# Performance work log

Hardware: AMD Instinct MI355X
Metric: run time of the kernel (lower is better)

The kernel has to match this reference:

```python
import jax, jax.numpy as jnp
import numpy as np

C64 = jnp.complex64
INV_SQRT2 = 1.0 / np.sqrt(2.0)
_H = jnp.array([[INV_SQRT2, INV_SQRT2], [INV_SQRT2, -INV_SQRT2]], dtype=C64)
_CNOT = jnp.array([[1, 0, 0, 0], [0, 1, 0, 0], [0, 0, 0, 1], [0, 0, 1, 0]], dtype=C64)  # wire0=control (index = 2*b0 + b1)


def _rz(t):
    # diag(e^{-it/2}, e^{it/2})
    return jnp.diag(jnp.stack([jnp.exp(-0.5j * t), jnp.exp(0.5j * t)]))


def _ry(t):
    c, s = jnp.cos(0.5 * t), jnp.sin(0.5 * t)
    return jnp.stack([jnp.stack([c, -s]), jnp.stack([s, c])]).astype(C64)


def _phase(p):
    # diag(1, e^{ip})
    return jnp.diag(jnp.stack([jnp.ones((), C64), jnp.exp(1j * p)]))


def _layer_unitary(p):
    # p: [14] already clipped. Gate order: CNOT -> H x H -> PhaseShift -> Rot(r,0,phi_s)=RZ(r+phi_s)
    #   -> Rot(r,phi_d,0)=RY(phi_d)@RZ(r) -> CPhase(k0)*CPhase(k1) = diag(1,1,1,e^{i(k0+k1)}).
    # bs_theta (p[0]) and bs_phi (p[1]) are computed but never used in a gate, matching the source.
    P = jnp.kron(_phase(p[2]), _phase(p[3]))
    S = jnp.kron(_rz(p[4] + p[6]), _rz(p[5] + p[7]))
    D = jnp.kron(_ry(p[10]) @ _rz(p[8]), _ry(p[11]) @ _rz(p[9]))
    CP = jnp.diag(jnp.stack([jnp.ones((), C64), jnp.ones((), C64), jnp.ones((), C64),
                             jnp.exp(1j * (p[12] + p[13]))]))
    HH = jnp.kron(_H, _H)
    return CP @ D @ S @ P @ HH @ _CNOT


def _total_unitary(params):
    # params: [L, 14]. FraudLayerParameters.__post_init__ clips everything to +-5 (kerr to +-1).
    p = jnp.concatenate([jnp.clip(params[:, :12], -5.0, 5.0),
                         jnp.clip(params[:, 12:], -1.0, 1.0)], axis=1)
    U = jnp.eye(4, dtype=C64)
    for i in range(params.shape[0]):  # static, tiny layer count
        U = _layer_unitary(p[i]) @ U
    return U


def setup_inputs() -> dict:
    key = jax.random.key(0)
    k1, k2, k3, k4 = jax.random.split(key, 4)
    B, n_layers, n_classes = 4194304, 3, 1  # layer 0 = input layer, layers 1..2 = variational
    x = jax.random.normal(k1, (B, 2), dtype=jnp.float32)
    params = jax.random.uniform(k2, (n_layers, 14), dtype=jnp.float32, minval=-1.0, maxval=1.0)
    W = jax.random.normal(k3, (n_classes, 1), dtype=jnp.float32)
    b = jax.random.normal(k4, (n_classes,), dtype=jnp.float32)
    return {"x": x, "params": params, "W": W, "b": b}


def reference(x, params, W, b):
    U = _total_unitary(params)  # constant 4x4 (params don't depend on the sample)
    h = 0.5 * x
    c, s = jnp.cos(h), jnp.sin(h)
    # RX(t)|0> = [cos(t/2), -i sin(t/2)]
    a0 = jnp.stack([c[:, 0].astype(C64), (-1j) * s[:, 0].astype(C64)], axis=-1)  # [B,2]
    a1 = jnp.stack([c[:, 1].astype(C64), (-1j) * s[:, 1].astype(C64)], axis=-1)  # [B,2]
    state = (a0[:, :, None] * a1[:, None, :]).reshape(-1, 4)  # kron, index = 2*b0 + b1
    psi = state @ U.T  # [B,4] = einsum('ij,bj->bi')
    prob = jnp.real(psi * jnp.conj(psi))  # [B,4]
    z_sign = jnp.array([1.0, 1.0, -1.0, -1.0], dtype=jnp.float32)  # <Z on wire 0>
    logits = (prob @ z_sign)[:, None]  # [B,1]
    return logits @ W.T + b  # [B, n_classes]
```

## Files before the change

kernel.cpp:

```cpp
#include <hip/hip_runtime.h>
#include <math.h>


__device__ inline void delem(float r, float phid, int a, int b,
                             float& outr, float& outi) {
    float sn, cs; __sincosf(0.5f * r, &sn, &cs);
    float sd, cd; __sincosf(0.5f * phid, &sd, &cd);
    float f = (a == b) ? cd : ((a == 1) ? sd : -sd);
    outr = f * cs;
    outi = f * ((b == 1) ? sn : -sn);
}

__device__ inline void cmatmul_shfl(float Ar, float Ai, float Br, float Bi,
                                    int i, int j, float& Cr, float& Ci) {
    float cr = 0.f, ci = 0.f;
    #pragma unroll
    for (int k = 0; k < 4; ++k) {
        float ar = __shfl(Ar, 4 * i + k, 64);
        float ai = __shfl(Ai, 4 * i + k, 64);
        float br = __shfl(Br, 4 * k + j, 64);
        float bi = __shfl(Bi, 4 * k + j, 64);
        cr = fmaf(ar, br, fmaf(-ai, bi, cr));
        ci = fmaf(ar, bi, fmaf(ai, br, ci));
    }
    Cr = cr; Ci = ci;
}

__device__ inline float eval_sample(float x0, float x1,
                                    float k00, float k01, float k02,
                                    float k10, float k11, float k12,
                                    float k20, float k21, float k22) {
    float s0, c0, s1, c1;
    __sincosf(x0, &s0, &c0);
    __sincosf(x1, &s1, &c1);
    float e0 = fmaf(s1, k02, fmaf(c1, k01, k00));
    float e1 = fmaf(s1, k12, fmaf(c1, k11, k10));
    float e2 = fmaf(s1, k22, fmaf(c1, k21, k20));
    return fmaf(s0, e2, fmaf(c0, e1, e0));
}

__global__ __launch_bounds__(256) void fraud_fused(
        const float* __restrict__ params, int n_layers,
        const float* __restrict__ W, const float* __restrict__ bias,
        const float4* __restrict__ x, float4* __restrict__ out, int nquads) {
    __shared__ float Am[16];

    const int t = threadIdx.x;

    if (t < 64) {
        const int i = (t >> 2) & 3, j = t & 3;
        const int i0 = i >> 1, i1 = i & 1, j0 = j >> 1, j1 = j & 1;

        float Ur = (i == j) ? 1.f : 0.f, Ui = 0.f;

        for (int l = 0; l < n_layers; ++l) {
            float p[14];
            #pragma unroll
            for (int q = 0; q < 14; ++q) {
                float v = params[l * 14 + q];
                float lim = (q < 12) ? 5.0f : 1.0f;
                p[q] = fminf(fmaxf(v, -lim), lim);
            }

            int sj = j ^ (j >> 1);
            float hh = (__popc(i & sj) & 1) ? -0.5f : 0.5f;
            float t0 = p[4] + p[6], t1 = p[5] + p[7];
            float th = p[2] * (float)i0 + p[3] * (float)i1
                     + 0.5f * t0 * (float)(2 * i0 - 1)
                     + 0.5f * t1 * (float)(2 * i1 - 1);
            float sth, cth; __sincosf(th, &sth, &cth);
            float Er = hh * cth, Ei = hh * sth;

            float ar, ai, br, bi;
            delem(p[8], p[10], i0, j0, ar, ai);
            delem(p[9], p[11], i1, j1, br, bi);
            float D4r = ar * br - ai * bi;
            float D4i = ar * bi + ai * br;

            float Lr, Li;
            cmatmul_shfl(D4r, D4i, Er, Ei, i, j, Lr, Li);
            if (i == 3) {
                float cps, cpc; __sincosf(p[12] + p[13], &cps, &cpc);
                float nr = Lr * cpc - Li * cps;
                float ni = Lr * cps + Li * cpc;
                Lr = nr; Li = ni;
            }

            if (l == 0) { Ur = Lr; Ui = Li; }
            else {
                float nr, ni;
                cmatmul_shfl(Lr, Li, Ur, Ui, i, j, nr, ni);
                Ur = nr; Ui = ni;
            }
        }

        float mr = 0.f, mi = 0.f;
        #pragma unroll
        for (int k = 0; k < 4; ++k) {
            float z = (k < 2) ? 1.f : -1.f;
            float u1r =  __shfl(Ur, 4 * k + i, 64);
            float u1i = -__shfl(Ui, 4 * k + i, 64);
            float u2r =  __shfl(Ur, 4 * k + j, 64);
            float u2i =  __shfl(Ui, 4 * k + j, 64);
            mr += z * (u1r * u2r - u1i * u2i);
            mi += z * (u1r * u2i + u1i * u2r);
        }
        float dri = (i == 0) ? 1.f : ((i == 3) ? -1.f : 0.f);
        float dii = (i == 0 || i == 3) ? 0.f : -1.f;
        float drj = (j == 0) ? 1.f : ((j == 3) ? -1.f : 0.f);
        float dij = (j == 0 || j == 3) ? 0.f : -1.f;
        float fr = dri * drj + dii * dij;
        float fi = dri * dij - dii * drj;
        if (t < 16) Am[t] = mr * fr - mi * fi;
    }
    __syncthreads();

    float A00 = Am[0],  A01 = Am[1],  A02 = Am[2],  A03 = Am[3];
    float A11 = Am[5],  A12 = Am[6],  A13 = Am[7];
    float A22 = Am[10], A23 = Am[11], A33 = Am[15];
    float w = W[0], bb = bias[0];
    float k00 = 0.25f * (A00 + A11 + A22 + A33) * w + bb;
    float k01 = 0.25f * (A00 - A11 + A22 - A33) * w;
    float k02 = 0.5f  * (A01 + A23) * w;
    float k10 = 0.25f * (A00 + A11 - A22 - A33) * w;
    float k11 = 0.25f * (A00 - A11 - A22 + A33) * w;
    float k12 = 0.5f  * (A01 - A23) * w;
    float k20 = 0.5f  * (A02 + A13) * w;
    float k21 = 0.5f  * (A02 - A13) * w;
    float k22 = 0.5f  * (A03 + A12) * w;

    const int gsize = gridDim.x * 256;
    for (int q = blockIdx.x * 256 + t; q < nquads; q += gsize) {
        float4 xa = x[2 * q];
        float4 xb = x[2 * q + 1];
        float4 o;
        o.x = eval_sample(xa.x, xa.y, k00, k01, k02, k10, k11, k12, k20, k21, k22);
        o.y = eval_sample(xa.z, xa.w, k00, k01, k02, k10, k11, k12, k20, k21, k22);
        o.z = eval_sample(xb.x, xb.y, k00, k01, k02, k10, k11, k12, k20, k21, k22);
        o.w = eval_sample(xb.z, xb.w, k00, k01, k02, k10, k11, k12, k20, k21, k22);
        out[q] = o;
    }
}

extern "C" void kernel_launch(void* const* d_in, const int* in_sizes, int n_in,
                              void* d_out, int out_size, void* d_ws, size_t ws_size,
                              hipStream_t stream) {
    const float* x      = (const float*)d_in[0];
    const float* params = (const float*)d_in[1];
    const float* W      = (const float*)d_in[2];
    const float* b      = (const float*)d_in[3];
    float* out = (float*)d_out;

    int n_layers = in_sizes[1] / 14;
    int B = out_size;
    int nq = B / 4;

    int blocks = 2048;
    int maxb = (nq + 255) / 256;
    if (blocks > maxb) blocks = maxb;

    fraud_fused<<<blocks, 256, 0, stream>>>(params, n_layers, W, b,
                                            (const float4*)x, (float4*)out, nq);
}
```

Before: 15.18 us.

## Prefetch first two sample quads before unitary setup and drop one shuffle matmul

Issues the global loads for each thread's first two quads of samples before the per-block 4x4 unitary computation and the barrier, so memory latency overlaps the setup math. The per-layer D·E product is now computed directly from local sincos values rather than through a shuffle-based matmul, which removes cross-lane shuffles at the cost of four sincos calls per element. The grid is sized to about two quads per thread, capped at 2048 blocks. This raises register pressure because the prefetched data stays live across the setup phase.

```diff
diff --git a/kernel.cpp b/kernel.cpp
--- a/kernel.cpp
+++ b/kernel.cpp
@@ -1,30 +1,6 @@
 #include <hip/hip_runtime.h>
 #include <math.h>
 
-
-__device__ inline void delem(float r, float phid, int a, int b,
-                             float& outr, float& outi) {
-    float sn, cs; __sincosf(0.5f * r, &sn, &cs);
-    float sd, cd; __sincosf(0.5f * phid, &sd, &cd);
-    float f = (a == b) ? cd : ((a == 1) ? sd : -sd);
-    outr = f * cs;
-    outi = f * ((b == 1) ? sn : -sn);
-}
-
-__device__ inline void cmatmul_shfl(float Ar, float Ai, float Br, float Bi,
-                                    int i, int j, float& Cr, float& Ci) {
-    float cr = 0.f, ci = 0.f;
-    #pragma unroll
-    for (int k = 0; k < 4; ++k) {
-        float ar = __shfl(Ar, 4 * i + k, 64);
-        float ai = __shfl(Ai, 4 * i + k, 64);
-        float br = __shfl(Br, 4 * k + j, 64);
-        float bi = __shfl(Bi, 4 * k + j, 64);
-        cr = fmaf(ar, br, fmaf(-ai, bi, cr));
-        ci = fmaf(ar, bi, fmaf(ai, br, ci));
-    }
-    Cr = cr; Ci = ci;
-}
 
 __device__ inline float eval_sample(float x0, float x1,
                                     float k00, float k01, float k02,
@@ -46,10 +22,19 @@
     __shared__ float Am[16];
 
     const int t = threadIdx.x;
+    const int gsize = gridDim.x * 256;
+    const int q0 = blockIdx.x * 256 + t;
+    const int q1 = q0 + gsize;
+    const bool v0 = q0 < nquads, v1 = q1 < nquads;
+
+    float4 xa0, xb0, xa1, xb1;
+    if (v0) { xa0 = x[2 * q0]; xb0 = x[2 * q0 + 1]; }
+    if (v1) { xa1 = x[2 * q1]; xb1 = x[2 * q1 + 1]; }
+    const float w = W[0], bb = bias[0];
 
     if (t < 64) {
         const int i = (t >> 2) & 3, j = t & 3;
-        const int i0 = i >> 1, i1 = i & 1, j0 = j >> 1, j1 = j & 1;
+        const int i0 = i >> 1, i1 = i & 1;
 
         float Ur = (i == j) ? 1.f : 0.f, Ui = 0.f;
 
@@ -57,28 +42,43 @@
             float p[14];
             #pragma unroll
             for (int q = 0; q < 14; ++q) {
-                float v = params[l * 14 + q];
+                float vv = params[l * 14 + q];
                 float lim = (q < 12) ? 5.0f : 1.0f;
-                p[q] = fminf(fmaxf(v, -lim), lim);
+                p[q] = fminf(fmaxf(vv, -lim), lim);
             }
+            float t0 = p[4] + p[6], t1 = p[5] + p[7];
+
+            float sn8,  cs8;  __sincosf(0.5f * p[8],  &sn8,  &cs8);
+            float sd10, cd10; __sincosf(0.5f * p[10], &sd10, &cd10);
+            float sn9,  cs9;  __sincosf(0.5f * p[9],  &sn9,  &cs9);
+            float sd11, cd11; __sincosf(0.5f * p[11], &sd11, &cd11);
+            float mag00 = (i0 == 0) ?  cd10 : sd10;
+            float mag01 = (i0 == 0) ? -sd10 : cd10;
+            float d00r = mag00 * cs8, d00i = -mag00 * sn8;
+            float d01r = mag01 * cs8, d01i =  mag01 * sn8;
+            float mag10 = (i1 == 0) ?  cd11 : sd11;
+            float mag11 = (i1 == 0) ? -sd11 : cd11;
+            float e10r = mag10 * cs9, e10i = -mag10 * sn9;
+            float e11r = mag11 * cs9, e11i =  mag11 * sn9;
 
             int sj = j ^ (j >> 1);
-            float hh = (__popc(i & sj) & 1) ? -0.5f : 0.5f;
-            float t0 = p[4] + p[6], t1 = p[5] + p[7];
-            float th = p[2] * (float)i0 + p[3] * (float)i1
-                     + 0.5f * t0 * (float)(2 * i0 - 1)
-                     + 0.5f * t1 * (float)(2 * i1 - 1);
-            float sth, cth; __sincosf(th, &sth, &cth);
-            float Er = hh * cth, Ei = hh * sth;
-
-            float ar, ai, br, bi;
-            delem(p[8], p[10], i0, j0, ar, ai);
-            delem(p[9], p[11], i1, j1, br, bi);
-            float D4r = ar * br - ai * bi;
-            float D4i = ar * bi + ai * br;
-
-            float Lr, Li;
-            cmatmul_shfl(D4r, D4i, Er, Ei, i, j, Lr, Li);
+            float Lr = 0.f, Li = 0.f;
+            #pragma unroll
+            for (int k = 0; k < 4; ++k) {
+                int k0 = k >> 1, k1 = k & 1;
+                float ar = k0 ? d01r : d00r, ai = k0 ? d01i : d00i;
+                float br = k1 ? e11r : e10r, bi = k1 ? e11i : e10i;
+                float Dr = ar * br - ai * bi;
+                float Di = ar * bi + ai * br;
+                float th = p[2] * (float)k0 + p[3] * (float)k1
+                         + 0.5f * t0 * (float)(2 * k0 - 1)
+                         + 0.5f * t1 * (float)(2 * k1 - 1);
+                float sth, cth; __sincosf(th, &sth, &cth);
+                float hh = (__popc(k & sj) & 1) ? -0.5f : 0.5f;
+                float Er2 = hh * cth, Ei2 = hh * sth;
+                Lr += Dr * Er2 - Di * Ei2;
+                Li += Dr * Ei2 + Di * Er2;
+            }
             if (i == 3) {
                 float cps, cpc; __sincosf(p[12] + p[13], &cps, &cpc);
                 float nr = Lr * cpc - Li * cps;
@@ -88,8 +88,16 @@
 
             if (l == 0) { Ur = Lr; Ui = Li; }
             else {
-                float nr, ni;
-                cmatmul_shfl(Lr, Li, Ur, Ui, i, j, nr, ni);
+                float nr = 0.f, ni = 0.f;
+                #pragma unroll
+                for (int k = 0; k < 4; ++k) {
+                    float ar = __shfl(Lr, 4 * i + k, 64);
+                    float ai = __shfl(Li, 4 * i + k, 64);
+                    float br = __shfl(Ur, 4 * k + j, 64);
+                    float bi = __shfl(Ui, 4 * k + j, 64);
+                    nr = fmaf(ar, br, fmaf(-ai, bi, nr));
+                    ni = fmaf(ar, bi, fmaf(ai, br, ni));
+                }
                 Ur = nr; Ui = ni;
             }
         }
@@ -118,7 +126,6 @@
     float A00 = Am[0],  A01 = Am[1],  A02 = Am[2],  A03 = Am[3];
     float A11 = Am[5],  A12 = Am[6],  A13 = Am[7];
     float A22 = Am[10], A23 = Am[11], A33 = Am[15];
-    float w = W[0], bb = bias[0];
     float k00 = 0.25f * (A00 + A11 + A22 + A33) * w + bb;
     float k01 = 0.25f * (A00 - A11 + A22 - A33) * w;
     float k02 = 0.5f  * (A01 + A23) * w;
@@ -129,8 +136,23 @@
     float k21 = 0.5f  * (A02 - A13) * w;
     float k22 = 0.5f  * (A03 + A12) * w;
 
-    const int gsize = gridDim.x * 256;
-    for (int q = blockIdx.x * 256 + t; q < nquads; q += gsize) {
+    if (v0) {
+        float4 o;
+        o.x = eval_sample(xa0.x, xa0.y, k00, k01, k02, k10, k11, k12, k20, k21, k22);
+        o.y = eval_sample(xa0.z, xa0.w, k00, k01, k02, k10, k11, k12, k20, k21, k22);
+        o.z = eval_sample(xb0.x, xb0.y, k00, k01, k02, k10, k11, k12, k20, k21, k22);
+        o.w = eval_sample(xb0.z, xb0.w, k00, k01, k02, k10, k11, k12, k20, k21, k22);
+        out[q0] = o;
+    }
+    if (v1) {
+        float4 o;
+        o.x = eval_sample(xa1.x, xa1.y, k00, k01, k02, k10, k11, k12, k20, k21, k22);
+        o.y = eval_sample(xa1.z, xa1.w, k00, k01, k02, k10, k11, k12, k20, k21, k22);
+        o.z = eval_sample(xb1.x, xb1.y, k00, k01, k02, k10, k11, k12, k20, k21, k22);
+        o.w = eval_sample(xb1.z, xb1.w, k00, k01, k02, k10, k11, k12, k20, k21, k22);
+        out[q1] = o;
+    }
+    for (int q = q1 + gsize; q < nquads; q += gsize) {
         float4 xa = x[2 * q];
         float4 xb = x[2 * q + 1];
         float4 o;
@@ -155,9 +177,8 @@
     int B = out_size;
     int nq = B / 4;
 
-    int blocks = 2048;
-    int maxb = (nq + 255) / 256;
-    if (blocks > maxb) blocks = maxb;
+    int blocks = (nq + 511) / 512;
+    if (blocks > 2048) blocks = 2048;
 
     fraud_fused<<<blocks, 256, 0, stream>>>(params, n_layers, W, b,
                                             (const float4*)x, (float4*)out, nq);
```

New measurement: 15.19 us. Within noise of the previous version (+0.1%).
